# Kernel tuning notes

Hardware: AMD Instinct MI355X
Metric: run time of the kernel (lower is better)

## Reference

```python
import jax, jax.numpy as jnp
import numpy as np


def setup_inputs() -> dict:
    key = jax.random.key(0)
    k1, k2, k3 = jax.random.split(key, 3)
    B, H, S, D, NPOS = 2, 16, 2048, 64, 64
    query = jax.random.normal(k1, (B, H, S, D), dtype=jnp.float32)
    attn_logits = jax.random.normal(k2, (B, H, S, S), dtype=jnp.float32)
    pos_emb = jax.random.normal(k3, (1, D, NPOS), dtype=jnp.float32)
    return {"query": query, "attn_logits": attn_logits, "pos_emb": pos_emb}


def reference(query, attn_logits, pos_emb):
    npos_max = pos_emb.shape[-1]
    # gated reverse-cumsum positions: [B,H,S,S]
    gates = jax.nn.sigmoid(attn_logits)
    pos = jnp.flip(jnp.cumsum(jnp.flip(gates, axis=-1), axis=-1), axis=-1)
    pos = jnp.minimum(pos, jnp.asarray(npos_max - 1, dtype=pos.dtype))
    pos_floor = jnp.floor(pos)
    idx_ceil = jnp.ceil(pos).astype(jnp.int32)
    idx_floor = pos_floor.astype(jnp.int32)
    # interpolation logits over learned positions: [B,H,S,npos_max]
    logits_int = jnp.einsum("bhsd,dn->bhsn", query, pos_emb[0])
    logits_ceil = jnp.take_along_axis(logits_int, idx_ceil, axis=-1)
    logits_floor = jnp.take_along_axis(logits_int, idx_floor, axis=-1)
    w = pos - pos_floor
    return logits_ceil * w + logits_floor * (1.0 - w)
```

## Files before the change

### kernel.cpp

```cpp
#include <hip/hip_runtime.h>


#define SLEN 2048
#define DDIM 64
#define NPOSN 64
#define ROWS (2 * 16 * 2048)

typedef float vfloat4 __attribute__((ext_vector_type(4)));

__global__ __launch_bounds__(256) void cope_kernel(
    const float* __restrict__ q,
    const float* __restrict__ attn,
    const float* __restrict__ emb,
    float* __restrict__ out)
{
    const int lane = threadIdx.x & 63;
    const int wave = threadIdx.x >> 6;
    const int r = blockIdx.x * 4 + wave;

    const float qv = q[(size_t)r * DDIM + lane];
    float lv = 0.0f;
    #pragma unroll
    for (int d = 0; d < DDIM; ++d)
        lv = fmaf(__shfl(qv, d), emb[d * NPOSN + lane], lv);
    const float l63 = __shfl(lv, NPOSN - 1);

    const float* __restrict__ arow = attn + (size_t)r * SLEN;
    float* __restrict__ orow = out + (size_t)r * SLEN;

    float carry = 0.0f;
    int jb = SLEN;
    while (jb > 0) {
        jb -= 64;
        const float x = arow[jb + lane];
        const float g = 1.0f / (1.0f + __expf(-x));
        float s = g;
        #pragma unroll
        for (int off = 1; off < 64; off <<= 1) {
            const float t = __shfl_down(s, off);
            if (lane + off < 64) s += t;
        }
        const float pos = fminf(carry + s, 63.0f);
        const float pf  = floorf(pos);
        const float w   = pos - pf;
        const float lf  = __shfl(lv, (int)pf);
        const float lc  = __shfl(lv, (int)ceilf(pos));
        __builtin_nontemporal_store(lc * w + lf * (1.0f - w), orow + jb + lane);
        carry += __shfl(s, 0);
        if (carry >= 63.0f) break;
    }

    const vfloat4 v4 = { l63, l63, l63, l63 };
    for (int j = lane * 4; j < jb; j += 256)
        __builtin_nontemporal_store(v4, reinterpret_cast<vfloat4*>(orow + j));
}

extern "C" void kernel_launch(void* const* d_in, const int* in_sizes, int n_in,
                              void* d_out, int out_size, void* d_ws, size_t ws_size,
                              hipStream_t stream) {
    const float* q    = (const float*)d_in[0];
    const float* attn = (const float*)d_in[1];
    const float* emb  = (const float*)d_in[2];
    float* out = (float*)d_out;

    dim3 grid(ROWS / 4), block(256);
    cope_kernel<<<grid, block, 0, stream>>>(q, attn, emb, out);
}
```

Before: 105.4 us.

## Process four rows per wave and prefetch first three attention chunks upfront

Each wavefront now handles four rows instead of one. It issues nontemporal loads for the last three 64-element chunks of every row before computing the query-embedding dot products, so memory latency overlaps with compute. The three chunks are scanned with interleaved shuffles, and the serial loop only continues if the carry has not yet saturated. The dot product now reads q directly instead of broadcasting it through shuffles. The grid shrinks by a factor of four, which lowers parallelism and raises register use.

```diff
diff --git a/kernel.cpp b/kernel.cpp
--- a/kernel.cpp
+++ b/kernel.cpp
@@ -5,8 +5,13 @@
 #define DDIM 64
 #define NPOSN 64
 #define ROWS (2 * 16 * 2048)
+#define RPW 4
 
 typedef float vfloat4 __attribute__((ext_vector_type(4)));
+
+__device__ __forceinline__ float sigmoidf_(float x) {
+    return 1.0f / (1.0f + __expf(-x));
+}
 
 __global__ __launch_bounds__(256) void cope_kernel(
     const float* __restrict__ q,
@@ -16,43 +21,100 @@
 {
     const int lane = threadIdx.x & 63;
     const int wave = threadIdx.x >> 6;
-    const int r = blockIdx.x * 4 + wave;
+    const int r0 = (blockIdx.x * 4 + wave) * RPW;
 
-    const float qv = q[(size_t)r * DDIM + lane];
-    float lv = 0.0f;
+    float c[RPW][3];
     #pragma unroll
-    for (int d = 0; d < DDIM; ++d)
-        lv = fmaf(__shfl(qv, d), emb[d * NPOSN + lane], lv);
-    const float l63 = __shfl(lv, NPOSN - 1);
+    for (int i = 0; i < RPW; ++i) {
+        const float* __restrict__ arow = attn + (size_t)(r0 + i) * SLEN;
+        c[i][0] = __builtin_nontemporal_load(arow + SLEN -  64 + lane);
+        c[i][1] = __builtin_nontemporal_load(arow + SLEN - 128 + lane);
+        c[i][2] = __builtin_nontemporal_load(arow + SLEN - 192 + lane);
+    }
 
-    const float* __restrict__ arow = attn + (size_t)r * SLEN;
-    float* __restrict__ orow = out + (size_t)r * SLEN;
+    float lv[RPW];
+    #pragma unroll
+    for (int i = 0; i < RPW; ++i) {
+        const float* __restrict__ qrow = q + (size_t)(r0 + i) * DDIM;
+        float a0 = 0.0f, a1 = 0.0f;
+        #pragma unroll
+        for (int d = 0; d < DDIM; d += 2) {
+            a0 = fmaf(qrow[d],     emb[d * NPOSN + lane],       a0);
+            a1 = fmaf(qrow[d + 1], emb[(d + 1) * NPOSN + lane], a1);
+        }
+        lv[i] = a0 + a1;
+    }
 
-    float carry = 0.0f;
-    int jb = SLEN;
-    while (jb > 0) {
-        jb -= 64;
-        const float x = arow[jb + lane];
-        const float g = 1.0f / (1.0f + __expf(-x));
-        float s = g;
+    #pragma unroll
+    for (int i = 0; i < RPW; ++i) {
+        const float lvi = lv[i];
+        float* __restrict__ orow = out + (size_t)(r0 + i) * SLEN;
+
+        float s0 = sigmoidf_(c[i][0]);
+        float s1 = sigmoidf_(c[i][1]);
+        float s2 = sigmoidf_(c[i][2]);
         #pragma unroll
         for (int off = 1; off < 64; off <<= 1) {
-            const float t = __shfl_down(s, off);
-            if (lane + off < 64) s += t;
+            const float t0 = __shfl_down(s0, off);
+            const float t1 = __shfl_down(s1, off);
+            const float t2 = __shfl_down(s2, off);
+            if (lane + off < 64) { s0 += t0; s1 += t1; s2 += t2; }
         }
-        const float pos = fminf(carry + s, 63.0f);
-        const float pf  = floorf(pos);
-        const float w   = pos - pf;
-        const float lf  = __shfl(lv, (int)pf);
-        const float lc  = __shfl(lv, (int)ceilf(pos));
-        __builtin_nontemporal_store(lc * w + lf * (1.0f - w), orow + jb + lane);
-        carry += __shfl(s, 0);
-        if (carry >= 63.0f) break;
+        const float T0 = __shfl(s0, 0);
+        const float T1 = __shfl(s1, 0);
+        const float T2 = __shfl(s2, 0);
+
+        {
+            const float pos = fminf(s0, 63.0f);
+            const float pf = floorf(pos), w = pos - pf;
+            const float lf = __shfl(lvi, (int)pf);
+            const float lc = __shfl(lvi, (int)ceilf(pos));
+            __builtin_nontemporal_store(lc * w + lf * (1.0f - w),
+                                        orow + SLEN - 64 + lane);
+        }
+        {
+            const float pos = fminf(T0 + s1, 63.0f);
+            const float pf = floorf(pos), w = pos - pf;
+            const float lf = __shfl(lvi, (int)pf);
+            const float lc = __shfl(lvi, (int)ceilf(pos));
+            __builtin_nontemporal_store(lc * w + lf * (1.0f - w),
+                                        orow + SLEN - 128 + lane);
+        }
+        {
+            const float pos = fminf(T0 + T1 + s2, 63.0f);
+            const float pf = floorf(pos), w = pos - pf;
+            const float lf = __shfl(lvi, (int)pf);
+            const float lc = __shfl(lvi, (int)ceilf(pos));
+            __builtin_nontemporal_store(lc * w + lf * (1.0f - w),
+                                        orow + SLEN - 192 + lane);
+        }
+
+        float carry = T0 + T1 + T2;
+        int jb = SLEN - 192;
+
+        const float* __restrict__ arow = attn + (size_t)(r0 + i) * SLEN;
+        while (carry < 63.0f && jb > 0) {
+            jb -= 64;
+            float s = sigmoidf_(arow[jb + lane]);
+            #pragma unroll
+            for (int off = 1; off < 64; off <<= 1) {
+                const float t = __shfl_down(s, off);
+                if (lane + off < 64) s += t;
+            }
+            const float pos = fminf(carry + s, 63.0f);
+            const float pf = floorf(pos), w = pos - pf;
+            const float lf = __shfl(lvi, (int)pf);
+            const float lc = __shfl(lvi, (int)ceilf(pos));
+            __builtin_nontemporal_store(lc * w + lf * (1.0f - w),
+                                        orow + jb + lane);
+            carry += __shfl(s, 0);
+        }
+
+        const float l63 = __shfl(lvi, NPOSN - 1);
+        const vfloat4 v4 = { l63, l63, l63, l63 };
+        for (int j = lane * 4; j < jb; j += 256)
+            __builtin_nontemporal_store(v4, reinterpret_cast<vfloat4*>(orow + j));
     }
-
-    const vfloat4 v4 = { l63, l63, l63, l63 };
-    for (int j = lane * 4; j < jb; j += 256)
-        __builtin_nontemporal_store(v4, reinterpret_cast<vfloat4*>(orow + j));
 }
 
 extern "C" void kernel_launch(void* const* d_in, const int* in_sizes, int n_in,
@@ -63,6 +125,6 @@
     const float* emb  = (const float*)d_in[2];
     float* out = (float*)d_out;
 
-    dim3 grid(ROWS / 4), block(256);
+    dim3 grid(ROWS / (4 * RPW)), block(256);
     cope_kernel<<<grid, block, 0, stream>>>(q, attn, emb, out);
 }
```

After: 137.6 us. +30.6%, slower.

## Process 256-element float4 chunks per wave and stage pos_emb in LDS

Applied to the files above, without the earlier changes.

Each wave now handles 256 attention values per iteration, with a float4 load per lane. The reverse cumsum runs within each thread's four elements before the wave scan, so one wave-level scan covers four times as many elements. The first chunk is prefetched before the query·pos_emb dot product, and pos_emb is copied into shared memory once per block. Early exit now happens at 256-element granularity, so a few extra sigmoids may be computed past the saturation point.

```diff
diff --git a/kernel.cpp b/kernel.cpp
--- a/kernel.cpp
+++ b/kernel.cpp
@@ -5,8 +5,13 @@
 #define DDIM 64
 #define NPOSN 64
 #define ROWS (2 * 16 * 2048)
+#define CH 256
 
 typedef float vfloat4 __attribute__((ext_vector_type(4)));
+
+__device__ __forceinline__ float sigmoidf_(float x) {
+    return 1.0f / (1.0f + __expf(-x));
+}
 
 __global__ __launch_bounds__(256) void cope_kernel(
     const float* __restrict__ q,
@@ -14,40 +19,83 @@
     const float* __restrict__ emb,
     float* __restrict__ out)
 {
+    __shared__ float semb[DDIM * NPOSN];
+    {
+        const float4* __restrict__ src = (const float4*)emb;
+        float4* __restrict__ dst = (float4*)semb;
+        #pragma unroll
+        for (int t = 0; t < 4; ++t)
+            dst[threadIdx.x + 256 * t] = src[threadIdx.x + 256 * t];
+    }
+    __syncthreads();
+
     const int lane = threadIdx.x & 63;
     const int wave = threadIdx.x >> 6;
-    const int r = blockIdx.x * 4 + wave;
+    const int r_u = __builtin_amdgcn_readfirstlane(blockIdx.x * 4 + wave);
 
-    const float qv = q[(size_t)r * DDIM + lane];
-    float lv = 0.0f;
+    const float* __restrict__ arow = attn + (size_t)r_u * SLEN;
+    float* __restrict__ orow = out + (size_t)r_u * SLEN;
+
+    float4 cur = *reinterpret_cast<const float4*>(arow + SLEN - CH + lane * 4);
+
+    const float* __restrict__ qrow = q + (size_t)r_u * DDIM;
+    float a0 = 0.0f, a1 = 0.0f;
     #pragma unroll
-    for (int d = 0; d < DDIM; ++d)
-        lv = fmaf(__shfl(qv, d), emb[d * NPOSN + lane], lv);
+    for (int d = 0; d < DDIM; d += 2) {
+        a0 = fmaf(qrow[d],     semb[d * NPOSN + lane],       a0);
+        a1 = fmaf(qrow[d + 1], semb[(d + 1) * NPOSN + lane], a1);
+    }
+    const float lv  = a0 + a1;
     const float l63 = __shfl(lv, NPOSN - 1);
-
-    const float* __restrict__ arow = attn + (size_t)r * SLEN;
-    float* __restrict__ orow = out + (size_t)r * SLEN;
 
     float carry = 0.0f;
     int jb = SLEN;
-    while (jb > 0) {
-        jb -= 64;
-        const float x = arow[jb + lane];
-        const float g = 1.0f / (1.0f + __expf(-x));
-        float s = g;
+    for (;;) {
+        const int base = jb - CH;
+        const float g0 = sigmoidf_(cur.x);
+        const float g1 = sigmoidf_(cur.y);
+        const float g2 = sigmoidf_(cur.z);
+        const float g3 = sigmoidf_(cur.w);
+        const float l3 = g3;
+        const float l2 = g2 + l3;
+        const float l1 = g1 + l2;
+        const float l0 = g0 + l1;
+        float s = l0;
         #pragma unroll
         for (int off = 1; off < 64; off <<= 1) {
             const float t = __shfl_down(s, off);
             if (lane + off < 64) s += t;
         }
-        const float pos = fminf(carry + s, 63.0f);
-        const float pf  = floorf(pos);
-        const float w   = pos - pf;
-        const float lf  = __shfl(lv, (int)pf);
-        const float lc  = __shfl(lv, (int)ceilf(pos));
-        __builtin_nontemporal_store(lc * w + lf * (1.0f - w), orow + jb + lane);
-        carry += __shfl(s, 0);
-        if (carry >= 63.0f) break;
+        const float excl = carry + (s - l0);
+        const float T    = __shfl(s, 0);
+
+        vfloat4 o;
+        {
+            const float pos = fminf(excl + l0, 63.0f);
+            const float pf = floorf(pos), w = pos - pf;
+            o.x = __shfl(lv, (int)ceilf(pos)) * w + __shfl(lv, (int)pf) * (1.0f - w);
+        }
+        {
+            const float pos = fminf(excl + l1, 63.0f);
+            const float pf = floorf(pos), w = pos - pf;
+            o.y = __shfl(lv, (int)ceilf(pos)) * w + __shfl(lv, (int)pf) * (1.0f - w);
+        }
+        {
+            const float pos = fminf(excl + l2, 63.0f);
+            const float pf = floorf(pos), w = pos - pf;
+            o.z = __shfl(lv, (int)ceilf(pos)) * w + __shfl(lv, (int)pf) * (1.0f - w);
+        }
+        {
+            const float pos = fminf(excl + l3, 63.0f);
+            const float pf = floorf(pos), w = pos - pf;
+            o.w = __shfl(lv, (int)ceilf(pos)) * w + __shfl(lv, (int)pf) * (1.0f - w);
+        }
+        __builtin_nontemporal_store(o, reinterpret_cast<vfloat4*>(orow + base + lane * 4));
+
+        carry += T;
+        jb = base;
+        if (carry >= 63.0f || jb == 0) break;
+        cur = *reinterpret_cast<const float4*>(arow + jb - CH + lane * 4);
     }
 
     const vfloat4 v4 = { l63, l63, l63, l63 };
```

After: 101.5 us. 3.7% less time.
